# Performance work log

Measured on AMD Instinct MI355X. Metric: run time of the kernel, lower is better.

Reference implementation:

```python
import jax, jax.numpy as jnp
import numpy as np

D_MODEL, N_HEADS, D_HEAD = 1024, 16, 64
INIT_RANGE = 0.02
IGNORE = -100000.0


def setup_inputs() -> dict:
    key = jax.random.key(0)
    ks = jax.random.split(key, 5)
    x = jax.random.normal(ks[0], (2, 2048, D_MODEL), dtype=jnp.float32)
    W_Q = jax.random.normal(ks[1], (N_HEADS, D_MODEL, D_HEAD), dtype=jnp.float32) * INIT_RANGE
    W_K = jax.random.normal(ks[2], (N_HEADS, D_MODEL, D_HEAD), dtype=jnp.float32) * INIT_RANGE
    W_V = jax.random.normal(ks[3], (N_HEADS, D_MODEL, D_HEAD), dtype=jnp.float32) * INIT_RANGE
    W_O = jax.random.normal(ks[4], (N_HEADS, D_HEAD, D_MODEL), dtype=jnp.float32) * INIT_RANGE
    b_Q = jnp.zeros((N_HEADS, D_HEAD), dtype=jnp.float32)
    b_K = jnp.zeros((N_HEADS, D_HEAD), dtype=jnp.float32)
    b_V = jnp.zeros((N_HEADS, D_HEAD), dtype=jnp.float32)
    b_O = jnp.zeros((D_MODEL,), dtype=jnp.float32)
    return {"normalized_resid_pre": x, "W_Q": W_Q, "b_Q": b_Q, "W_K": W_K,
            "b_K": b_K, "W_V": W_V, "b_V": b_V, "W_O": W_O, "b_O": b_O}


def reference(normalized_resid_pre, W_Q, b_Q, W_K, b_K, W_V, b_V, W_O, b_O):
    x = normalized_resid_pre  # [b, s, d_model]
    q = jnp.einsum('bsd,hde->bshe', x, W_Q) + b_Q  # [b, s, h, d_head]
    k = jnp.einsum('bsd,hde->bshe', x, W_K) + b_K
    v = jnp.einsum('bsd,hde->bshe', x, W_V) + b_V
    scores = jnp.einsum('bqhe,bkhe->bhqk', q, k) / jnp.sqrt(jnp.float32(D_HEAD))
    S = scores.shape[-1]
    causal = jnp.triu(jnp.ones((S, S), dtype=bool), k=1)  # True above diagonal
    scores = jnp.where(causal, jnp.float32(IGNORE), scores)
    pattern = jax.nn.softmax(scores, axis=-1)
    z = jnp.einsum('bhqk,bkhe->bqhe', pattern, v)
    out = jnp.einsum('bqhe,hed->bqd', z, W_O) + b_O
    return out
```

## Files before the change

### kernel.cpp

```cpp
#include <hip/hip_runtime.h>
#include <math.h>

#define DMODEL 1024
#define NHEADS 16
#define DHEAD 64
#define SEQL 2048
#define NBATCH 2
#define MROWS (NBATCH*SEQL)
#define NQKV (3*DMODEL)

typedef __attribute__((ext_vector_type(8))) short bf8;
typedef __attribute__((ext_vector_type(4))) float f4;
typedef __attribute__((ext_vector_type(16))) float f16v;

__device__ __forceinline__ unsigned short f2b(float f) {
  union { float f; unsigned int u; } v; v.f = f;
  unsigned int r = v.u + 0x7FFFu + ((v.u >> 16) & 1u);
  return (unsigned short)(r >> 16);
}

__device__ __forceinline__ f4 mfma16(bf8 a, bf8 b, f4 c) {
  return __builtin_amdgcn_mfma_f32_16x16x32_bf16(a, b, c, 0, 0, 0);
}

__device__ __forceinline__ f16v mfma32(bf8 a, bf8 b, f16v c) {
  return __builtin_amdgcn_mfma_f32_32x32x16_bf16(a, b, c, 0, 0, 0);
}

__device__ __forceinline__ unsigned cvtpk(float lo, float hi) {
  unsigned r;
  asm("v_cvt_pk_bf16_f32 %0, %1, %2" : "=v"(r) : "v"(lo), "v"(hi));
  return r;
}

__device__ __forceinline__ void gload16(const void* g, void* l) {
  __builtin_amdgcn_global_load_lds(
      (const __attribute__((address_space(1))) unsigned int*)g,
      (__attribute__((address_space(3))) unsigned int*)l, 16, 0, 0);
}


__global__ __launch_bounds__(256) void k_f32_to_bf16(const float* __restrict__ in,
                                                     unsigned short* __restrict__ out, int n4) {
  int i = blockIdx.x * 256 + threadIdx.x;
  if (i < n4) {
    float4 v = ((const float4*)in)[i];
    ushort4 o;
    o.x = f2b(v.x); o.y = f2b(v.y); o.z = f2b(v.z); o.w = f2b(v.w);
    ((ushort4*)out)[i] = o;
  }
}

__global__ __launch_bounds__(256) void k_pack_wqkv(
    const float* __restrict__ Wq, const float* __restrict__ Wk, const float* __restrict__ Wv,
    const float* __restrict__ bq, const float* __restrict__ bk, const float* __restrict__ bv,
    unsigned short* __restrict__ Wt, float* __restrict__ biasq) {
  __shared__ float tile[64][65];
  int tid = threadIdx.x;
  int dt = blockIdx.x, h = blockIdx.y, p = blockIdx.z;
  const float* W = (p == 0) ? Wq : ((p == 1) ? Wk : Wv);
  #pragma unroll
  for (int j = 0; j < 16; j++) {
    int idx = tid + j * 256;
    int dd = idx >> 6, e = idx & 63;
    tile[dd][e] = W[(size_t)(h * DMODEL + dt * 64 + dd) * DHEAD + e];
  }
  __syncthreads();
  #pragma unroll
  for (int j = 0; j < 16; j++) {
    int idx = tid + j * 256;
    int e = idx >> 6, dd = idx & 63;
    Wt[(size_t)(p * DMODEL + h * 64 + e) * DMODEL + dt * 64 + dd] = f2b(tile[dd][e]);
  }
  if (dt == 0 && tid < 64) {
    const float* bsel = (p == 0) ? bq : ((p == 1) ? bk : bv);
    biasq[p * DMODEL + h * 64 + tid] = bsel[h * 64 + tid];
  }
}

__global__ __launch_bounds__(256) void k_pack_wo(const float* __restrict__ Wo,
                                                 unsigned short* __restrict__ Wot) {
  __shared__ float tile[64][65];
  int tid = threadIdx.x;
  int het = blockIdx.x, dmt = blockIdx.y;
  #pragma unroll
  for (int j = 0; j < 16; j++) {
    int idx = tid + j * 256;
    int r = idx >> 6, c = idx & 63;
    tile[r][c] = Wo[(size_t)(het * 64 + r) * DMODEL + dmt * 64 + c];
  }
  __syncthreads();
  #pragma unroll
  for (int j = 0; j < 16; j++) {
    int idx = tid + j * 256;
    int rr = idx >> 6, cc = idx & 63;
    Wot[(size_t)(dmt * 64 + rr) * DMODEL + het * 64 + cc] = f2b(tile[cc][rr]);
  }
}


template<int N, int K, bool OUTF32>
__global__ __launch_bounds__(256) void k_gemm_bt(
    const unsigned short* __restrict__ A, const unsigned short* __restrict__ Bt,
    const float* __restrict__ bias, void* __restrict__ Cp) {
  __shared__ unsigned short As[128 * 64];
  __shared__ unsigned short Bs[128 * 64];
  int tid = threadIdx.x;
  int lane = tid & 63, w = tid >> 6;
  int wr = w >> 1, wc = w & 1;
  int lr = lane & 15, lg = lane >> 4;
  int m0 = blockIdx.x * 128, n0 = blockIdx.y * 128;
  int srow = w * 8 + (lane >> 3);
  int scol = ((lane & 7) ^ (lane >> 3)) * 8;
  f4 acc[4][4] = {};
  for (int k0 = 0; k0 < K; k0 += 64) {
    #pragma unroll
    for (int it = 0; it < 4; it++) {
      int row = it * 32 + srow;
      gload16(&A[(size_t)(m0 + row) * K + k0 + scol], &As[(it * 256 + w * 64) * 8]);
      gload16(&Bt[(size_t)(n0 + row) * K + k0 + scol], &Bs[(it * 256 + w * 64) * 8]);
    }
    __syncthreads();
    #pragma unroll
    for (int kk = 0; kk < 2; kk++) {
      bf8 af[4], bfv[4];
      #pragma unroll
      for (int i = 0; i < 4; i++) {
        int ra = wr * 64 + i * 16 + lr;
        int rb = wc * 64 + i * 16 + lr;
        af[i]  = *(const bf8*)(&As[ra * 64 + (((kk * 4 + lg) ^ (ra & 7)) * 8)]);
        bfv[i] = *(const bf8*)(&Bs[rb * 64 + (((kk * 4 + lg) ^ (rb & 7)) * 8)]);
      }
      #pragma unroll
      for (int i = 0; i < 4; i++)
        #pragma unroll
        for (int j = 0; j < 4; j++)
          acc[i][j] = mfma16(af[i], bfv[j], acc[i][j]);
    }
    __syncthreads();
  }
  #pragma unroll
  for (int i = 0; i < 4; i++)
    #pragma unroll
    for (int j = 0; j < 4; j++) {
      int col = n0 + wc * 64 + j * 16 + lr;
      float bv = bias[col];
      #pragma unroll
      for (int r = 0; r < 4; r++) {
        int row = m0 + wr * 64 + i * 16 + lg * 4 + r;
        float v = acc[i][j][r] + bv;
        if (OUTF32) ((float*)Cp)[(size_t)row * N + col] = v;
        else ((unsigned short*)Cp)[(size_t)row * N + col] = f2b(v);
      }
    }
}


#define VKP 72
#define VSWZ(r, c) ((r) * VKP + ((c) ^ ((((r) >> 3) & 7) << 3)))

__global__ __launch_bounds__(256, 2) void k_attn(const unsigned short* __restrict__ qkv,
                                                 unsigned short* __restrict__ zb) {
  __shared__ __align__(16) unsigned short Ks[64 * 64];
  __shared__ __align__(16) unsigned short Vt[64 * VKP];
  __shared__ float Lb[4][32];
  int tid = threadIdx.x;
  int lane = tid & 63, w = tid >> 6;
  int l31 = lane & 31, h5 = lane >> 5;
  int qt = 15 - blockIdx.x;
  int bh = blockIdx.y;
  int b = bh >> 4, h = bh & 15;
  int qw = qt * 128 + w * 32;
  const size_t rowbase = (size_t)b * SEQL;
  int qg = qw + l31;

  bf8 qf[4];
  #pragma unroll
  for (int ds = 0; ds < 4; ds++)
    qf[ds] = *(const bf8*)(&qkv[(rowbase + qg) * NQKV + h * DHEAD + ds * 16 + h5 * 8]);

  f16v zacc0 = {}, zacc1 = {};
  float m = -1e30f, lsum = 0.f;

  int sr = tid >> 3;
  int scc = ((tid & 7) ^ (sr & 7)) * 8;

  int nkv = 2 * qt + 2;
  for (int tt = 0; tt < nkv; tt++) {
    int kv0 = tt * 64;
    #pragma unroll
    for (int it = 0; it < 2; it++)
      gload16(&qkv[(rowbase + kv0 + it * 32 + sr) * NQKV + DMODEL + h * DHEAD + scc],
              &Ks[(it * 256 + w * 64) * 8]);
    #pragma unroll
    for (int cc = 0; cc < 2; cc++) {
      int c = tid + cc * 256;
      int kv = c >> 3, dc = (c & 7) * 8;
      int4 vvi = *(const int4*)(&qkv[(rowbase + kv0 + kv) * NQKV + 2 * DMODEL + h * DHEAD + dc]);
      const unsigned short* vv = (const unsigned short*)&vvi;
      #pragma unroll
      for (int i2 = 0; i2 < 8; i2++) Vt[VSWZ(dc + i2, kv)] = vv[i2];
    }
    __syncthreads();
    #pragma unroll
    for (int t32 = 0; t32 < 2; t32++) {
      int kb = kv0 + t32 * 32;
      if (kb <= qw + 31) {
        f16v sa = {};
        int ar = t32 * 32 + l31;
        #pragma unroll
        for (int ds = 0; ds < 4; ds++) {
          bf8 kf = *(const bf8*)(&Ks[ar * 64 + (((ds * 2 + h5) ^ (ar & 7)) * 8)]);
          sa = mfma32(kf, qf[ds], sa);
        }
        float p[16];
        int diffh = qg - kb - 4 * h5;
        if (kb + 31 > qw) {
          #pragma unroll
          for (int r = 0; r < 16; r++) {
            int kc4 = (r & 3) + 8 * (r >> 2);
            p[r] = (kc4 > diffh) ? -1e30f : sa[r] * 0.125f;
          }
        } else {
          #pragma unroll
          for (int r = 0; r < 16; r++) p[r] = sa[r] * 0.125f;
        }
        float pmax = p[0];
        #pragma unroll
        for (int r = 1; r < 16; r++) pmax = fmaxf(pmax, p[r]);
        pmax = fmaxf(pmax, __shfl_xor(pmax, 32));
        if (!__all(pmax - m <= 8.0f)) {
          float mn = fmaxf(m, pmax);
          float al = __expf(m - mn);
          Lb[w][l31] = al;
          m = mn;
          lsum *= al;
          #pragma unroll
          for (int r = 0; r < 16; r++) {
            float alr = Lb[w][(r & 3) + 8 * (r >> 2) + 4 * h5];
            zacc0[r] *= alr;
            zacc1[r] *= alr;
          }
        }
        float ps = 0.f;
        #pragma unroll
        for (int r = 0; r < 16; r++) { p[r] = __expf(p[r] - m); ps += p[r]; }
        ps += __shfl_xor(ps, 32);
        lsum += ps;
        unsigned X1 = cvtpk(p[0], p[1]),   Y1 = cvtpk(p[4], p[5]);
        unsigned X2 = cvtpk(p[2], p[3]),   Y2 = cvtpk(p[6], p[7]);
        unsigned X3 = cvtpk(p[8], p[9]),   Y3 = cvtpk(p[12], p[13]);
        unsigned X4 = cvtpk(p[10], p[11]), Y4 = cvtpk(p[14], p[15]);
        unsigned Xs1 = __shfl_xor((int)X1, 32), Ys1 = __shfl_xor((int)Y1, 32);
        unsigned Xs2 = __shfl_xor((int)X2, 32), Ys2 = __shfl_xor((int)Y2, 32);
        unsigned Xs3 = __shfl_xor((int)X3, 32), Ys3 = __shfl_xor((int)Y3, 32);
        unsigned Xs4 = __shfl_xor((int)X4, 32), Ys4 = __shfl_xor((int)Y4, 32);
        union { bf8 v; unsigned u[4]; } pa0, pa1;
        pa0.u[0] = h5 ? Ys1 : X1;  pa0.u[2] = h5 ? Y1 : Xs1;
        pa0.u[1] = h5 ? Ys2 : X2;  pa0.u[3] = h5 ? Y2 : Xs2;
        pa1.u[0] = h5 ? Ys3 : X3;  pa1.u[2] = h5 ? Y3 : Xs3;
        pa1.u[1] = h5 ? Ys4 : X4;  pa1.u[3] = h5 ? Y4 : Xs4;
        #pragma unroll
        for (int e = 0; e < 2; e++) {
          int vr = e * 32 + l31;
          int fv = ((vr >> 3) & 7) << 3;
          f16v& zr = e ? zacc1 : zacc0;
          #pragma unroll
          for (int ks = 0; ks < 2; ks++) {
            bf8 vb = *(const bf8*)(&Vt[vr * VKP + ((t32 * 32 + ks * 16 + h5 * 8) ^ fv)]);
            zr = mfma32(ks ? pa1.v : pa0.v, vb, zr);
          }
        }
      }
    }
    __syncthreads();
  }
  Lb[w][l31] = 1.0f / lsum;
  #pragma unroll
  for (int r = 0; r < 16; r++) {
    int crow = (r & 3) + 8 * (r >> 2) + 4 * h5;
    float inv = Lb[w][crow];
    size_t row = rowbase + qw + crow;
    zb[row * DMODEL + h * DHEAD + l31] = f2b(zacc0[r] * inv);
    zb[row * DMODEL + h * DHEAD + 32 + l31] = f2b(zacc1[r] * inv);
  }
}


extern "C" void kernel_launch(void* const* d_in, const int* in_sizes, int n_in,
                              void* d_out, int out_size, void* d_ws, size_t ws_size,
                              hipStream_t stream) {
  const float* x  = (const float*)d_in[0];
  const float* Wq = (const float*)d_in[1];
  const float* bq = (const float*)d_in[2];
  const float* Wk = (const float*)d_in[3];
  const float* bk = (const float*)d_in[4];
  const float* Wv = (const float*)d_in[5];
  const float* bv = (const float*)d_in[6];
  const float* Wo = (const float*)d_in[7];
  const float* bo = (const float*)d_in[8];

  char* ws = (char*)d_ws;
  unsigned short* xb    = (unsigned short*)(ws);
  unsigned short* wqkvt = (unsigned short*)(ws + 8388608);
  float*          biasq = (float*)(ws + 8388608 + 6291456);
  unsigned short* qkv   = (unsigned short*)(ws + 8388608 + 6291456 + 16384);
  unsigned short* wot   = (unsigned short*)(ws + 8388608 + 6291456 + 16384 + 25165824);
  unsigned short* zbuf  = xb;

  k_f32_to_bf16<<<(MROWS * DMODEL / 4 + 255) / 256, 256, 0, stream>>>(x, xb, MROWS * DMODEL / 4);
  k_pack_wqkv<<<dim3(16, 16, 3), 256, 0, stream>>>(Wq, Wk, Wv, bq, bk, bv, wqkvt, biasq);
  k_pack_wo<<<dim3(16, 16), 256, 0, stream>>>(Wo, wot);
  k_gemm_bt<NQKV, DMODEL, false><<<dim3(32, 24), 256, 0, stream>>>(xb, wqkvt, biasq, qkv);
  k_attn<<<dim3(16, 32), 256, 0, stream>>>(qkv, zbuf);
  k_gemm_bt<DMODEL, DMODEL, true><<<dim3(32, 8), 256, 0, stream>>>(zbuf, wot, bo, (float*)d_out);
}
```

Before: 232.2 us.

## Emit V pre-transposed from projection GEMM and double-buffer K/V tiles in attention

The QKV projection is split into a Q/K GEMM writing a 2048-wide buffer and a separate V GEMM whose epilogue writes V transposed ([b, d, s]) as bf16. Because V arrives already transposed, attention loads both K and V with async 16-byte global-to-LDS loads instead of scalar LDS transposes, and it double-buffers the K/V tiles so the next tile's loads overlap current compute. It also flips the q-tile order for batch 1 to balance load across blocks, and drops the occupancy hint of 2 in launch_bounds. In exchange there is an extra kernel launch, LDS use doubles, and the transposed-V epilogue does strided 8-byte stores.

After: 220.8 us. 4.9% less time.

```diff
diff --git a/kernel.cpp b/kernel.cpp
--- a/kernel.cpp
+++ b/kernel.cpp
@@ -7,7 +7,7 @@
 #define SEQL 2048
 #define NBATCH 2
 #define MROWS (NBATCH*SEQL)
-#define NQKV (3*DMODEL)
+#define QKS 2048
 
 typedef __attribute__((ext_vector_type(8))) short bf8;
 typedef __attribute__((ext_vector_type(4))) float f4;
@@ -99,7 +99,7 @@
 }
 
 
-template<int N, int K, bool OUTF32>
+template<int N, int K, int MODE>
 __global__ __launch_bounds__(256) void k_gemm_bt(
     const unsigned short* __restrict__ A, const unsigned short* __restrict__ Bt,
     const float* __restrict__ bias, void* __restrict__ Cp) {
@@ -139,37 +139,54 @@
     }
     __syncthreads();
   }
-  #pragma unroll
-  for (int i = 0; i < 4; i++)
-    #pragma unroll
-    for (int j = 0; j < 4; j++) {
-      int col = n0 + wc * 64 + j * 16 + lr;
-      float bv = bias[col];
-      #pragma unroll
-      for (int r = 0; r < 4; r++) {
-        int row = m0 + wr * 64 + i * 16 + lg * 4 + r;
-        float v = acc[i][j][r] + bv;
-        if (OUTF32) ((float*)Cp)[(size_t)row * N + col] = v;
-        else ((unsigned short*)Cp)[(size_t)row * N + col] = f2b(v);
-      }
-    }
-}
-
-
-#define VKP 72
-#define VSWZ(r, c) ((r) * VKP + ((c) ^ ((((r) >> 3) & 7) << 3)))
-
-__global__ __launch_bounds__(256, 2) void k_attn(const unsigned short* __restrict__ qkv,
-                                                 unsigned short* __restrict__ zb) {
-  __shared__ __align__(16) unsigned short Ks[64 * 64];
-  __shared__ __align__(16) unsigned short Vt[64 * VKP];
+  if (MODE == 2) {
+    #pragma unroll
+    for (int i = 0; i < 4; i++) {
+      int row0 = m0 + wr * 64 + i * 16 + lg * 4;
+      int b = row0 >> 11, s0 = row0 & 2047;
+      #pragma unroll
+      for (int j = 0; j < 4; j++) {
+        int col = n0 + wc * 64 + j * 16 + lr;
+        float bv = bias[col];
+        ushort4 o;
+        o.x = f2b(acc[i][j][0] + bv);
+        o.y = f2b(acc[i][j][1] + bv);
+        o.z = f2b(acc[i][j][2] + bv);
+        o.w = f2b(acc[i][j][3] + bv);
+        *(ushort4*)((unsigned short*)Cp + (size_t)(b * 1024 + col) * 2048 + s0) = o;
+      }
+    }
+  } else {
+    #pragma unroll
+    for (int i = 0; i < 4; i++)
+      #pragma unroll
+      for (int j = 0; j < 4; j++) {
+        int col = n0 + wc * 64 + j * 16 + lr;
+        float bv = bias[col];
+        #pragma unroll
+        for (int r = 0; r < 4; r++) {
+          int row = m0 + wr * 64 + i * 16 + lg * 4 + r;
+          float v = acc[i][j][r] + bv;
+          if (MODE == 1) ((float*)Cp)[(size_t)row * N + col] = v;
+          else ((unsigned short*)Cp)[(size_t)row * N + col] = f2b(v);
+        }
+      }
+  }
+}
+
+
+__global__ __launch_bounds__(256) void k_attn(const unsigned short* __restrict__ qkv2,
+                                              const unsigned short* __restrict__ vT,
+                                              unsigned short* __restrict__ zb) {
+  __shared__ __align__(16) unsigned short Ks[2][64 * 64];
+  __shared__ __align__(16) unsigned short Vs[2][64 * 64];
   __shared__ float Lb[4][32];
   int tid = threadIdx.x;
   int lane = tid & 63, w = tid >> 6;
   int l31 = lane & 31, h5 = lane >> 5;
-  int qt = 15 - blockIdx.x;
-  int bh = blockIdx.y;
-  int b = bh >> 4, h = bh & 15;
+  int bx = blockIdx.x, by = blockIdx.y;
+  int b = by >> 4, h = by & 15;
+  int qt = b ? bx : (15 - bx);
   int qw = qt * 128 + w * 32;
   const size_t rowbase = (size_t)b * SEQL;
   int qg = qw + l31;
@@ -177,7 +194,10 @@
   bf8 qf[4];
   #pragma unroll
   for (int ds = 0; ds < 4; ds++)
-    qf[ds] = *(const bf8*)(&qkv[(rowbase + qg) * NQKV + h * DHEAD + ds * 16 + h5 * 8]);
+    qf[ds] = *(const bf8*)(&qkv2[(rowbase + qg) * QKS + h * DHEAD + ds * 16 + h5 * 8]);
+
+  const unsigned short* Kg = qkv2 + DMODEL + h * DHEAD;
+  const unsigned short* Vg = vT + (size_t)(b * 1024 + h * DHEAD) * SEQL;
 
   f16v zacc0 = {}, zacc1 = {};
   float m = -1e30f, lsum = 0.f;
@@ -186,22 +206,25 @@
   int scc = ((tid & 7) ^ (sr & 7)) * 8;
 
   int nkv = 2 * qt + 2;
+  #pragma unroll
+  for (int it = 0; it < 2; it++) {
+    gload16(&Kg[(rowbase + it * 32 + sr) * QKS + scc], &Ks[0][(it * 256 + w * 64) * 8]);
+    gload16(&Vg[(size_t)(it * 32 + sr) * SEQL + scc], &Vs[0][(it * 256 + w * 64) * 8]);
+  }
+  __syncthreads();
+  int buf = 0;
   for (int tt = 0; tt < nkv; tt++) {
+    if (tt + 1 < nkv) {
+      int kn = (tt + 1) * 64;
+      #pragma unroll
+      for (int it = 0; it < 2; it++) {
+        gload16(&Kg[(rowbase + kn + it * 32 + sr) * QKS + scc], &Ks[buf ^ 1][(it * 256 + w * 64) * 8]);
+        gload16(&Vg[(size_t)(it * 32 + sr) * SEQL + kn + scc], &Vs[buf ^ 1][(it * 256 + w * 64) * 8]);
+      }
+    }
     int kv0 = tt * 64;
-    #pragma unroll
-    for (int it = 0; it < 2; it++)
-      gload16(&qkv[(rowbase + kv0 + it * 32 + sr) * NQKV + DMODEL + h * DHEAD + scc],
-              &Ks[(it * 256 + w * 64) * 8]);
-    #pragma unroll
-    for (int cc = 0; cc < 2; cc++) {
-      int c = tid + cc * 256;
-      int kv = c >> 3, dc = (c & 7) * 8;
-      int4 vvi = *(const int4*)(&qkv[(rowbase + kv0 + kv) * NQKV + 2 * DMODEL + h * DHEAD + dc]);
-      const unsigned short* vv = (const unsigned short*)&vvi;
-      #pragma unroll
-      for (int i2 = 0; i2 < 8; i2++) Vt[VSWZ(dc + i2, kv)] = vv[i2];
-    }
-    __syncthreads();
+    const unsigned short* KsB = &Ks[buf][0];
+    const unsigned short* VsB = &Vs[buf][0];
     #pragma unroll
     for (int t32 = 0; t32 < 2; t32++) {
       int kb = kv0 + t32 * 32;
@@ -210,7 +233,7 @@
         int ar = t32 * 32 + l31;
         #pragma unroll
         for (int ds = 0; ds < 4; ds++) {
-          bf8 kf = *(const bf8*)(&Ks[ar * 64 + (((ds * 2 + h5) ^ (ar & 7)) * 8)]);
+          bf8 kf = *(const bf8*)(&KsB[ar * 64 + (((ds * 2 + h5) ^ (ar & 7)) * 8)]);
           sa = mfma32(kf, qf[ds], sa);
         }
         float p[16];
@@ -263,17 +286,17 @@
         #pragma unroll
         for (int e = 0; e < 2; e++) {
           int vr = e * 32 + l31;
-          int fv = ((vr >> 3) & 7) << 3;
           f16v& zr = e ? zacc1 : zacc0;
           #pragma unroll
           for (int ks = 0; ks < 2; ks++) {
-            bf8 vb = *(const bf8*)(&Vt[vr * VKP + ((t32 * 32 + ks * 16 + h5 * 8) ^ fv)]);
+            bf8 vb = *(const bf8*)(&VsB[vr * 64 + (((t32 * 4 + ks * 2 + h5) ^ (vr & 7)) * 8)]);
             zr = mfma32(ks ? pa1.v : pa0.v, vb, zr);
           }
         }
       }
     }
     __syncthreads();
+    buf ^= 1;
   }
   Lb[w][l31] = 1.0f / lsum;
   #pragma unroll
@@ -303,15 +326,18 @@
   char* ws = (char*)d_ws;
   unsigned short* xb    = (unsigned short*)(ws);
   unsigned short* wqkvt = (unsigned short*)(ws + 8388608);
-  float*          biasq = (float*)(ws + 8388608 + 6291456);
-  unsigned short* qkv   = (unsigned short*)(ws + 8388608 + 6291456 + 16384);
-  unsigned short* wot   = (unsigned short*)(ws + 8388608 + 6291456 + 16384 + 25165824);
+  float*          biasq = (float*)(ws + 14680064);
+  unsigned short* qkv2  = (unsigned short*)(ws + 14696448);
+  unsigned short* vT    = (unsigned short*)(ws + 31473664);
+  unsigned short* wot   = (unsigned short*)(ws + 39862272);
   unsigned short* zbuf  = xb;
 
   k_f32_to_bf16<<<(MROWS * DMODEL / 4 + 255) / 256, 256, 0, stream>>>(x, xb, MROWS * DMODEL / 4);
   k_pack_wqkv<<<dim3(16, 16, 3), 256, 0, stream>>>(Wq, Wk, Wv, bq, bk, bv, wqkvt, biasq);
   k_pack_wo<<<dim3(16, 16), 256, 0, stream>>>(Wo, wot);
-  k_gemm_bt<NQKV, DMODEL, false><<<dim3(32, 24), 256, 0, stream>>>(xb, wqkvt, biasq, qkv);
-  k_attn<<<dim3(16, 32), 256, 0, stream>>>(qkv, zbuf);
-  k_gemm_bt<DMODEL, DMODEL, true><<<dim3(32, 8), 256, 0, stream>>>(zbuf, wot, bo, (float*)d_out);
-}
+  k_gemm_bt<QKS, DMODEL, 0><<<dim3(32, 16), 256, 0, stream>>>(xb, wqkvt, biasq, qkv2);
+  k_gemm_bt<DMODEL, DMODEL, 2><<<dim3(32, 8), 256, 0, stream>>>(
+      xb, wqkvt + (size_t)2048 * DMODEL, biasq + 2048, vT);
+  k_attn<<<dim3(16, 32), 256, 0, stream>>>(qkv2, vT, zbuf);
+  k_gemm_bt<DMODEL, DMODEL, 1><<<dim3(32, 8), 256, 0, stream>>>(zbuf, wot, bo, (float*)d_out);
+}
```
